# Kernel optimization log

Measured on AMD Instinct MI355X. Metric: run time of the kernel, lower is better.

## Reference

```python
import jax, jax.numpy as jnp
import numpy as np

D = 1024
H = 8          # MHA fallback num_heads
DH = D // H
DFF = 4096     # mlp_ratio * hidden_size
EPS = 1e-6


def _ln(x, g, b):
    mu = jnp.mean(x, axis=-1, keepdims=True)
    var = jnp.mean((x - mu) ** 2, axis=-1, keepdims=True)
    return (x - mu) * jax.lax.rsqrt(var + EPS) * g + b


def setup_inputs() -> dict:
    key = jax.random.key(0)
    ks = jax.random.split(key, 16)
    s = 0.02
    return {
        "x": jax.random.normal(ks[0], (8, 1024, D), jnp.float32),
        "c": jax.random.normal(ks[1], (8, D), jnp.float32),
        # Mamba-block (attention fallback) params
        "m_ada_w": jax.random.normal(ks[2], (D, 3 * D), jnp.float32) * s,
        "m_ada_b": jnp.zeros((3 * D,), jnp.float32),
        "m_norm_g": jnp.ones((D,), jnp.float32),
        "m_norm_b": jnp.zeros((D,), jnp.float32),
        "in_proj_w": jax.random.normal(ks[3], (3 * D, D), jnp.float32) * s,
        "in_proj_b": jnp.zeros((3 * D,), jnp.float32),
        "out_proj_w": jax.random.normal(ks[4], (D, D), jnp.float32) * s,
        "out_proj_b": jnp.zeros((D,), jnp.float32),
        # FeedForward-block params
        "f_ada_w": jax.random.normal(ks[5], (D, 3 * D), jnp.float32) * s,
        "f_ada_b": jnp.zeros((3 * D,), jnp.float32),
        "f_norm_g": jnp.ones((D,), jnp.float32),
        "f_norm_b": jnp.zeros((D,), jnp.float32),
        "w1": jax.random.normal(ks[6], (D, DFF), jnp.float32) * s,
        "b1": jnp.zeros((DFF,), jnp.float32),
        "w2": jax.random.normal(ks[7], (DFF, D), jnp.float32) * s,
        "b2": jnp.zeros((D,), jnp.float32),
    }


def reference(x, c, m_ada_w, m_ada_b, m_norm_g, m_norm_b, in_proj_w, in_proj_b,
              out_proj_w, out_proj_b, f_ada_w, f_ada_b, f_norm_g, f_norm_b,
              w1, b1, w2, b2):
    B, N, _ = x.shape
    # ---- MambaBlock (MHA fallback), dropout = identity (eval) ----
    mod = jax.nn.silu(c) @ m_ada_w + m_ada_b              # (B, 3D)
    shift, scale, gate = jnp.split(mod, 3, axis=-1)
    h = _ln(x, m_norm_g, m_norm_b)
    h = h * (1.0 + scale[:, None, :]) + shift[:, None, :]
    qkv = h @ in_proj_w.T + in_proj_b                      # (B, N, 3D)
    q, k, v = jnp.split(qkv, 3, axis=-1)
    q = q.reshape(B, N, H, DH)
    k = k.reshape(B, N, H, DH)
    v = v.reshape(B, N, H, DH)
    scores = jnp.einsum("bqhd,bkhd->bhqk", q, k) / np.sqrt(DH).astype(np.float32)
    attn = jax.nn.softmax(scores, axis=-1)
    o = jnp.einsum("bhqk,bkhd->bqhd", attn, v).reshape(B, N, D)
    o = o @ out_proj_w.T + out_proj_b
    x = x + gate[:, None, :] * o
    # ---- FeedForward block ----
    mod2 = jax.nn.silu(c) @ f_ada_w + f_ada_b
    shift2, scale2, gate2 = jnp.split(mod2, 3, axis=-1)
    h = _ln(x, f_norm_g, f_norm_b)
    h = h * (1.0 + scale2[:, None, :]) + shift2[:, None, :]
    h = jax.nn.gelu(h @ w1 + b1, approximate=False) @ w2 + b2
    return x + gate2[:, None, :] * h
```

## Files before the change

### kernel.cpp

```cpp
#include <hip/hip_runtime.h>

typedef __bf16 bf16x8 __attribute__((ext_vector_type(8)));
typedef float f32x4 __attribute__((ext_vector_type(4)));

__device__ __forceinline__ unsigned short f2bf(float f) {
    unsigned int u = __float_as_uint(f);
    unsigned int r = (u + 0x7FFFu + ((u >> 16) & 1u)) >> 16;
    return (unsigned short)r;
}

__device__ __forceinline__ void gload16(const void* g, void* l) {
    __builtin_amdgcn_global_load_lds(
        (const __attribute__((address_space(1))) unsigned int*)g,
        (__attribute__((address_space(3))) unsigned int*)l, 16, 0, 0);
}

__device__ __forceinline__ void barrier_raw() {
    asm volatile("" ::: "memory");
    __builtin_amdgcn_s_barrier();
    asm volatile("" ::: "memory");
}

__device__ __forceinline__ void vmwait0() {
    asm volatile("s_waitcnt vmcnt(0)" ::: "memory");
}

__device__ __forceinline__ float gelu_fast(float u) {
    float z = 1.595769122f * u + 0.071354816f * u * u * u;
    return u / (1.f + __expf(-z));
}

__global__ __launch_bounds__(256) void f2b4(const float* __restrict__ in,
                                            unsigned short* __restrict__ out) {
    size_t i = ((size_t)blockIdx.x * 256 + threadIdx.x) * 4;
    float4 v = *(const float4*)(in + i);
    ushort4 o;
    o.x = f2bf(v.x); o.y = f2bf(v.y); o.z = f2bf(v.z); o.w = f2bf(v.w);
    *(ushort4*)(out + i) = o;
}

__global__ __launch_bounds__(256) void transpose_f2b(const float* __restrict__ in,
                                                     unsigned short* __restrict__ out,
                                                     int R, int C) {
    __shared__ float tile[32][33];
    int r0 = blockIdx.y * 32, c0 = blockIdx.x * 32;
    int tx = threadIdx.x & 31, ty = threadIdx.x >> 5;
#pragma unroll
    for (int i = 0; i < 4; i++) {
        int r = ty + i * 8;
        tile[r][tx] = in[(size_t)(r0 + r) * C + c0 + tx];
    }
    __syncthreads();
#pragma unroll
    for (int i = 0; i < 4; i++) {
        int r = ty + i * 8;
        out[(size_t)(c0 + r) * R + r0 + tx] = f2bf(tile[tx][r]);
    }
}

__global__ __launch_bounds__(256) void ada_mod_part(const float* __restrict__ c,
                                                    const float* __restrict__ W,
                                                    float* __restrict__ partial) {
    __shared__ float sc[8 * 64];
    int kc = blockIdx.y * 64;
    for (int i = threadIdx.x; i < 512; i += 256) {
        int b = i >> 6, k = i & 63;
        float cv = c[b * 1024 + kc + k];
        sc[i] = cv / (1.f + __expf(-cv));
    }
    __syncthreads();
    int j = blockIdx.x * 256 + threadIdx.x;
    float acc[8] = {0, 0, 0, 0, 0, 0, 0, 0};
    for (int k = 0; k < 64; k++) {
        float w = W[(size_t)(kc + k) * 3072 + j];
#pragma unroll
        for (int b = 0; b < 8; b++) acc[b] += sc[b * 64 + k] * w;
    }
#pragma unroll
    for (int b = 0; b < 8; b++) partial[((size_t)blockIdx.y * 8 + b) * 3072 + j] = acc[b];
}

__global__ __launch_bounds__(256) void ada_reduce(const float* __restrict__ partial,
                                                  const float* __restrict__ bias,
                                                  float* __restrict__ out) {
    int idx = blockIdx.x * 256 + threadIdx.x;
    int b = idx / 3072;
    int jj = idx - b * 3072;
    float s = bias[jj];
#pragma unroll
    for (int ch = 0; ch < 16; ch++) s += partial[((size_t)ch * 8 + b) * 3072 + jj];
    out[idx] = s;
}

__global__ __launch_bounds__(256) void ln_mod_kernel(const float* __restrict__ x,
                                                     const float* __restrict__ gamma,
                                                     const float* __restrict__ beta,
                                                     const float* __restrict__ mods,
                                                     unsigned short* __restrict__ out) {
    int row = blockIdx.x;
    int b = row >> 10;
    float4 v = ((const float4*)(x + (size_t)row * 1024))[threadIdx.x];
    float s = v.x + v.y + v.z + v.w;
    float s2 = v.x * v.x + v.y * v.y + v.z * v.z + v.w * v.w;
#pragma unroll
    for (int d = 1; d < 64; d <<= 1) { s += __shfl_xor(s, d); s2 += __shfl_xor(s2, d); }
    __shared__ float red[8];
    int lane = threadIdx.x & 63, wid = threadIdx.x >> 6;
    if (lane == 0) { red[wid] = s; red[4 + wid] = s2; }
    __syncthreads();
    float S = red[0] + red[1] + red[2] + red[3];
    float S2 = red[4] + red[5] + red[6] + red[7];
    float mu = S * (1.f / 1024.f);
    float var = S2 * (1.f / 1024.f) - mu * mu;
    float rs = rsqrtf(var + 1e-6f);
    const float* mrow = mods + b * 3072;
    int j0 = threadIdx.x * 4;
    float hv[4] = {v.x, v.y, v.z, v.w};
    ushort4 o;
    unsigned short* op = (unsigned short*)&o;
#pragma unroll
    for (int i = 0; i < 4; i++) {
        int j = j0 + i;
        float hh = (hv[i] - mu) * rs * gamma[j] + beta[j];
        hh = hh * (1.f + mrow[1024 + j]) + mrow[j];
        op[i] = f2bf(hh);
    }
    *(ushort4*)(out + (size_t)row * 1024 + j0) = o;
}

template <int EP>
__global__ __launch_bounds__(256, 2) void gemmw(const unsigned short* __restrict__ A,
                                                const unsigned short* __restrict__ Bt,
                                                int N, int K, int nx,
                                                const float* __restrict__ bias,
                                                unsigned short* __restrict__ outb,
                                                unsigned short* __restrict__ vt) {
    constexpr int AE = 128 * 32;
    constexpr int BE = 256 * 32;
    extern __shared__ __align__(16) char smem[];
    __bf16* As = (__bf16*)smem;
    __bf16* Bs = As + 3 * AE;

    int tid = threadIdx.x, lane = tid & 63, wid = tid >> 6;
    int t = lane & 15, g = lane >> 4;
    int xk2 = ((t >> 1) & 3) * 8;

    int nwg = gridDim.x, chunk = nwg >> 3;
    int swz = (blockIdx.x & 7) * chunk + (blockIdx.x >> 3);
    int bx = swz % nx, by = swz / nx;
    int rowA0 = by * 128, colB0 = bx * 256;

    int rin = tid >> 2, cblk = tid & 3;
    int scol = (cblk ^ ((rin >> 1) & 3)) * 8;

    auto stage = [&](int nb, int kt) {
        int k0 = kt << 5;
        gload16(A + (size_t)(rowA0 + rin) * K + k0 + scol, As + nb * AE + tid * 8);
        gload16(A + (size_t)(rowA0 + 64 + rin) * K + k0 + scol,
                As + nb * AE + 2048 + tid * 8);
#pragma unroll
        for (int sl = 0; sl < 4; sl++)
            gload16(Bt + (size_t)(colB0 + sl * 64 + rin) * K + k0 + scol,
                    Bs + nb * BE + sl * 2048 + tid * 8);
    };

    f32x4 acc[8][4];
#pragma unroll
    for (int m = 0; m < 8; m++)
#pragma unroll
        for (int n = 0; n < 4; n++) acc[m][n] = (f32x4){0.f, 0.f, 0.f, 0.f};

    int NT = K >> 5;
    stage(0, 0);
    if (NT > 1) {
        stage(1, 1);
        asm volatile("s_waitcnt vmcnt(6)" ::: "memory");
    } else {
        vmwait0();
    }
    barrier_raw();

    int cur = 0, tgt = 2;
#pragma unroll 1
    for (int kt = 0; kt < NT; ++kt) {
        bool deep = (kt + 2) < NT;
        bool more = (kt + 1) < NT;
        if (deep) stage(tgt, kt + 2);
        const __bf16* Ac = As + cur * AE;
        const __bf16* Bc = Bs + cur * BE;

        bf16x8 b[4];
#pragma unroll
        for (int n = 0; n < 4; n++)
            b[n] = *(const bf16x8*)&Bc[(wid * 64 + n * 16 + t) * 32 + ((g * 8) ^ xk2)];

        __builtin_amdgcn_s_setprio(1);
#pragma unroll
        for (int mh = 0; mh < 2; mh++) {
            bf16x8 a[4];
#pragma unroll
            for (int m4 = 0; m4 < 4; m4++)
                a[m4] = *(const bf16x8*)&Ac[(mh * 64 + m4 * 16 + t) * 32 + ((g * 8) ^ xk2)];
#pragma unroll
            for (int m4 = 0; m4 < 4; m4++)
#pragma unroll
                for (int n = 0; n < 4; n++)
                    acc[mh * 4 + m4][n] =
                        __builtin_amdgcn_mfma_f32_16x16x32_bf16(a[m4], b[n], acc[mh * 4 + m4][n], 0, 0, 0);
        }
        __builtin_amdgcn_s_setprio(0);

        if (more) {
            if (deep) {
                asm volatile("s_waitcnt vmcnt(6)" ::: "memory");
            } else {
                vmwait0();
            }
            barrier_raw();
        }
        cur = (cur == 2) ? 0 : cur + 1;
        tgt = (tgt == 2) ? 0 : tgt + 1;
    }

    int col0 = colB0 + wid * 64;
    bool vpart = (EP == 0) && (colB0 >= 2048);
#pragma unroll
    for (int m = 0; m < 8; m++)
#pragma unroll
        for (int n = 0; n < 4; n++) {
            int col = col0 + n * 16 + t;
            if (EP == 0 && vpart) {
                int hcol = col - 2048;
                int hh = hcol >> 7, d = hcol & 127;
                int bb = rowA0 >> 10;
                int ntok = (rowA0 + m * 16 + g * 4) & 1023;
                float bs = bias[col];
                ushort4 vv;
                vv.x = f2bf(acc[m][n][0] + bs);
                vv.y = f2bf(acc[m][n][1] + bs);
                vv.z = f2bf(acc[m][n][2] + bs);
                vv.w = f2bf(acc[m][n][3] + bs);
                *(ushort4*)(vt + (((size_t)(bb * 8 + hh) * 128 + d) * 1024 + ntok)) = vv;
            } else {
#pragma unroll
                for (int r = 0; r < 4; r++) {
                    int row = rowA0 + m * 16 + g * 4 + r;
                    float v = acc[m][n][r];
                    if (EP == 0) {
                        outb[(size_t)row * N + col] = f2bf(v + bias[col]);
                    } else {
                        outb[(size_t)row * N + col] = f2bf(gelu_fast(v + bias[col]));
                    }
                }
            }
        }
}

template <int EP>
__global__ __launch_bounds__(256, 4) void gemmo(const unsigned short* __restrict__ A,
                                                const unsigned short* __restrict__ Bt,
                                                int N, int K, int nx,
                                                const float* __restrict__ bias,
                                                const float* __restrict__ xres,
                                                const float* __restrict__ mods,
                                                float* __restrict__ outf) {
    constexpr int AE = 128 * 32;
    constexpr int BE = 128 * 32;
    extern __shared__ __align__(16) char smem[];
    __bf16* As = (__bf16*)smem;
    __bf16* Bs = As + 3 * AE;

    int tid = threadIdx.x, lane = tid & 63, wid = tid >> 6;
    int wr = wid >> 1, wc = wid & 1;
    int t = lane & 15, g = lane >> 4;
    int xk2 = ((t >> 1) & 3) * 8;

    int nwg = gridDim.x, chunk = nwg >> 3;
    int swz = (blockIdx.x & 7) * chunk + (blockIdx.x >> 3);
    int bx = swz % nx, by = swz / nx;
    int rowA0 = by * 128, colB0 = bx * 128;

    int rin = tid >> 2, cblk = tid & 3;
    int scol = (cblk ^ ((rin >> 1) & 3)) * 8;

    auto stage = [&](int nb, int kt) {
        int k0 = kt << 5;
        gload16(A + (size_t)(rowA0 + rin) * K + k0 + scol, As + nb * AE + tid * 8);
        gload16(A + (size_t)(rowA0 + 64 + rin) * K + k0 + scol,
                As + nb * AE + 2048 + tid * 8);
        gload16(Bt + (size_t)(colB0 + rin) * K + k0 + scol, Bs + nb * BE + tid * 8);
        gload16(Bt + (size_t)(colB0 + 64 + rin) * K + k0 + scol,
                Bs + nb * BE + 2048 + tid * 8);
    };

    f32x4 acc[4][4];
#pragma unroll
    for (int m = 0; m < 4; m++)
#pragma unroll
        for (int n = 0; n < 4; n++) acc[m][n] = (f32x4){0.f, 0.f, 0.f, 0.f};

    int NT = K >> 5;
    stage(0, 0);
    if (NT > 1) {
        stage(1, 1);
        asm volatile("s_waitcnt vmcnt(4)" ::: "memory");
    } else {
        vmwait0();
    }
    barrier_raw();

    int cur = 0, tgt = 2;
#pragma unroll 1
    for (int kt = 0; kt < NT; ++kt) {
        bool deep = (kt + 2) < NT;
        bool more = (kt + 1) < NT;
        if (deep) stage(tgt, kt + 2);
        const __bf16* Ac = As + cur * AE;
        const __bf16* Bc = Bs + cur * BE;

        bf16x8 a[4], b[4];
#pragma unroll
        for (int m = 0; m < 4; m++)
            a[m] = *(const bf16x8*)&Ac[(wr * 64 + m * 16 + t) * 32 + ((g * 8) ^ xk2)];
#pragma unroll
        for (int n = 0; n < 4; n++)
            b[n] = *(const bf16x8*)&Bc[(wc * 64 + n * 16 + t) * 32 + ((g * 8) ^ xk2)];

        __builtin_amdgcn_s_setprio(1);
#pragma unroll
        for (int m = 0; m < 4; m++)
#pragma unroll
            for (int n = 0; n < 4; n++)
                acc[m][n] = __builtin_amdgcn_mfma_f32_16x16x32_bf16(a[m], b[n], acc[m][n], 0, 0, 0);
        __builtin_amdgcn_s_setprio(0);

        if (more) {
            if (deep) {
                asm volatile("s_waitcnt vmcnt(4)" ::: "memory");
            } else {
                vmwait0();
            }
            barrier_raw();
        }
        cur = (cur == 2) ? 0 : cur + 1;
        tgt = (tgt == 2) ? 0 : tgt + 1;
    }

    int row0 = rowA0 + wr * 64, col0 = colB0 + wc * 64;
#pragma unroll
    for (int m = 0; m < 4; m++)
#pragma unroll
        for (int n = 0; n < 4; n++) {
            int col = col0 + n * 16 + t;
#pragma unroll
            for (int r = 0; r < 4; r++) {
                int row = row0 + m * 16 + g * 4 + r;
                float v = acc[m][n][r];
                int bb = row >> 10;
                float gt = mods[bb * 3072 + 2048 + col];
                if (EP == 1) {
                    outf[(size_t)row * 1024 + col] =
                        xres[(size_t)row * 1024 + col] + gt * (v + bias[col]);
                } else {
                    outf[(size_t)row * 1024 + col] += gt * (v + bias[col]);
                }
            }
        }
}

__global__ __launch_bounds__(512, 4) void attn_kernel(const unsigned short* __restrict__ qkv,
                                                      const unsigned short* __restrict__ vt,
                                                      unsigned short* __restrict__ o) {
    extern __shared__ __align__(16) char asmem[];
    __bf16* Ks = (__bf16*)asmem;
    __bf16* Vts = Ks + 2 * 64 * 128;

    int bid = blockIdx.x;
    int logical = (bid & 7) * 64 + (bid >> 3);
    int q0 = (logical & 7) * 128;
    int bh = logical >> 3;
    int b = bh >> 3, h = bh & 7;
    int tid = threadIdx.x, lane = tid & 63, w = tid >> 6;
    int t = lane & 15, g = lane >> 4;
    int swzt = (t & 7) << 4;

    const unsigned short* qbase = qkv + (size_t)(b * 1024) * 3072 + h * 128;
    int qrow = q0 + w * 16 + t;
    bf16x8 qf[4];
#pragma unroll
    for (int ks = 0; ks < 4; ks++)
        qf[ks] = *(const bf16x8*)(qbase + (size_t)qrow * 3072 + ks * 32 + g * 8);

    f32x4 Oa[8];
#pragma unroll
    for (int n = 0; n < 8; n++) Oa[n] = (f32x4){0.f, 0.f, 0.f, 0.f};
    float m_r = -1e30f, l_r = 0.f;
    const float scale = 0.08838834764831845f;

    int krow = tid >> 4;
    int ksrc = (((tid & 15) * 16) ^ ((krow & 7) << 4)) >> 1;
    int vrow = tid >> 3;
    int vsrc = (((tid & 7) * 16) ^ ((vrow & 7) << 4)) >> 1;
    const unsigned short* vtg = vt + (size_t)bh * 128 * 1024;

    auto stage = [&](int buf, int kv0) {
        const unsigned short* kb = qkv + (size_t)(b * 1024 + kv0) * 3072 + 1024 + h * 128;
#pragma unroll
        for (int cc = 0; cc < 2; cc++) {
            gload16(kb + (size_t)(cc * 32 + krow) * 3072 + ksrc,
                    (void*)(Ks + buf * 8192 + cc * 4096 + tid * 8));
            gload16(vtg + (size_t)(cc * 64 + vrow) * 1024 + kv0 + vsrc,
                    (void*)(Vts + buf * 8192 + cc * 4096 + tid * 8));
        }
    };

    stage(0, 0);
    vmwait0();
    barrier_raw();

#pragma unroll 1
    for (int tile = 0; tile < 16; ++tile) {
        int cur = tile & 1;
        bool more = tile < 15;
        if (more) stage(cur ^ 1, (tile + 1) * 64);
        const __bf16* Kc = Ks + cur * 8192;
        const __bf16* Vc = Vts + cur * 8192;

        f32x4 St[4];
#pragma unroll
        for (int n = 0; n < 4; n++) St[n] = (f32x4){0.f, 0.f, 0.f, 0.f};
        __builtin_amdgcn_s_setprio(1);
#pragma unroll
        for (int ks = 0; ks < 4; ks++) {
#pragma unroll
            for (int n = 0; n < 4; n++) {
                bf16x8 kf = *(const bf16x8*)&Kc[(n * 16 + t) * 128 + (((ks * 64 + g * 16) ^ swzt) >> 1)];
                St[n] = __builtin_amdgcn_mfma_f32_16x16x32_bf16(kf, qf[ks], St[n], 0, 0, 0);
            }
        }
        __builtin_amdgcn_s_setprio(0);

        float mx = -1e30f;
#pragma unroll
        for (int n = 0; n < 4; n++)
#pragma unroll
            for (int r = 0; r < 4; r++) mx = fmaxf(mx, St[n][r]);
        mx *= scale;
        mx = fmaxf(mx, __shfl_xor(mx, 16));
        mx = fmaxf(mx, __shfl_xor(mx, 32));
        float mn = fmaxf(m_r, mx);
        float alpha = __expf(m_r - mn);
        m_r = mn;
        float p[4][4];
        float rs = 0.f;
#pragma unroll
        for (int n = 0; n < 4; n++)
#pragma unroll
            for (int r = 0; r < 4; r++) {
                float pv = __expf(St[n][r] * scale - mn);
                p[n][r] = pv;
                rs += pv;
            }
        rs += __shfl_xor(rs, 16);
        rs += __shfl_xor(rs, 32);
        l_r = l_r * alpha + rs;

        unsigned P01[4], P23[4];
#pragma unroll
        for (int n = 0; n < 4; n++) {
            P01[n] = (unsigned)f2bf(p[n][0]) | ((unsigned)f2bf(p[n][1]) << 16);
            P23[n] = (unsigned)f2bf(p[n][2]) | ((unsigned)f2bf(p[n][3]) << 16);
        }

#pragma unroll
        for (int r = 0; r < 4; r++) {
            float ar = __shfl(alpha, (lane & 48) + g * 4 + r);
#pragma unroll
            for (int n2 = 0; n2 < 8; n2++) Oa[n2][r] *= ar;
        }

#pragma unroll
        for (int ks2 = 0; ks2 < 2; ks2++) {
            int e = ks2 * 2, od = ks2 * 2 + 1;
            unsigned s16a = (g < 2) ? P01[e] : P01[od];
            unsigned s16b = (g < 2) ? P23[e] : P23[od];
            unsigned s32a = (g & 1) ? P01[e] : P01[od];
            unsigned s32b = (g & 1) ? P23[e] : P23[od];
            unsigned s48a = (g >= 2) ? P01[e] : P01[od];
            unsigned s48b = (g >= 2) ? P23[e] : P23[od];
            unsigned r16a = __shfl_xor(s16a, 16), r16b = __shfl_xor(s16b, 16);
            unsigned r32a = __shfl_xor(s32a, 32), r32b = __shfl_xor(s32b, 32);
            unsigned r48a = __shfl_xor(s48a, 48), r48b = __shfl_xor(s48b, 48);
            union { unsigned u[4]; bf16x8 v; } pa;
            pa.u[0] = (g == 0) ? P01[e] : (g == 1) ? r48a : (g == 2) ? r32a : r16a;
            pa.u[1] = (g == 0) ? P23[e] : (g == 1) ? r48b : (g == 2) ? r32b : r16b;
            pa.u[2] = (g == 0) ? r16a : (g == 1) ? r32a : (g == 2) ? r48a : P01[od];
            pa.u[3] = (g == 0) ? r16b : (g == 1) ? r32b : (g == 2) ? r48b : P23[od];
            __builtin_amdgcn_s_setprio(1);
#pragma unroll
            for (int n2 = 0; n2 < 8; n2++) {
                bf16x8 vf = *(const bf16x8*)&Vc[(n2 * 16 + t) * 64 + (((ks2 * 64 + g * 16) ^ swzt) >> 1)];
                Oa[n2] = __builtin_amdgcn_mfma_f32_16x16x32_bf16(pa.v, vf, Oa[n2], 0, 0, 0);
            }
            __builtin_amdgcn_s_setprio(0);
        }

        if (more) {
            vmwait0();
            barrier_raw();
        }
    }

#pragma unroll
    for (int r = 0; r < 4; r++) {
        float lq = __shfl(l_r, (lane & 48) + g * 4 + r);
        float inv = 1.f / lq;
        int orow = q0 + w * 16 + g * 4 + r;
#pragma unroll
        for (int n2 = 0; n2 < 8; n2++)
            o[(size_t)(b * 1024 + orow) * 1024 + h * 128 + n2 * 16 + t] = f2bf(Oa[n2][r] * inv);
    }
}

extern "C" void kernel_launch(void* const* d_in, const int* in_sizes, int n_in,
                              void* d_out, int out_size, void* d_ws, size_t ws_size,
                              hipStream_t stream) {
    const float* x          = (const float*)d_in[0];
    const float* c          = (const float*)d_in[1];
    const float* m_ada_w    = (const float*)d_in[2];
    const float* m_ada_b    = (const float*)d_in[3];
    const float* m_norm_g   = (const float*)d_in[4];
    const float* m_norm_b   = (const float*)d_in[5];
    const float* in_proj_w  = (const float*)d_in[6];
    const float* in_proj_b  = (const float*)d_in[7];
    const float* out_proj_w = (const float*)d_in[8];
    const float* out_proj_b = (const float*)d_in[9];
    const float* f_ada_w    = (const float*)d_in[10];
    const float* f_ada_b    = (const float*)d_in[11];
    const float* f_norm_g   = (const float*)d_in[12];
    const float* f_norm_b   = (const float*)d_in[13];
    const float* w1         = (const float*)d_in[14];
    const float* b1         = (const float*)d_in[15];
    const float* w2         = (const float*)d_in[16];
    const float* b2         = (const float*)d_in[17];
    float* out = (float*)d_out;
    char* ws = (char*)d_ws;

    unsigned short* Wq   = (unsigned short*)(ws + 0);
    unsigned short* Wo   = (unsigned short*)(ws + 6291456);
    unsigned short* vt   = (unsigned short*)(ws + 8388608);
    unsigned short* W1t  = (unsigned short*)(ws + 8388608);
    unsigned short* W2t  = (unsigned short*)(ws + 16777216);
    float*          modm = (float*)(ws + 25165824);
    float*          modf = (float*)(ws + 25264128);
    unsigned short* hbuf = (unsigned short*)(ws + 25362432);
    float*          part = (float*)(ws + 25362432);
    float*          part2= (float*)(ws + 25362432 + 2097152);
    unsigned short* qkv  = (unsigned short*)(ws + 42139648);
    unsigned short* obuf = (unsigned short*)(ws + 92471296);
    unsigned short* h2   = (unsigned short*)(ws + 42139648);

    hipFuncSetAttribute((const void*)&gemmw<0>, hipFuncAttributeMaxDynamicSharedMemorySize, 73728);
    hipFuncSetAttribute((const void*)&gemmw<2>, hipFuncAttributeMaxDynamicSharedMemorySize, 73728);
    hipFuncSetAttribute((const void*)&gemmo<1>, hipFuncAttributeMaxDynamicSharedMemorySize, 49152);
    hipFuncSetAttribute((const void*)&gemmo<3>, hipFuncAttributeMaxDynamicSharedMemorySize, 49152);
    hipFuncSetAttribute((const void*)&attn_kernel, hipFuncAttributeMaxDynamicSharedMemorySize, 65536);

    hipLaunchKernelGGL(ada_mod_part, dim3(12, 16), dim3(256), 0, stream, c, m_ada_w, part);
    hipLaunchKernelGGL(ada_mod_part, dim3(12, 16), dim3(256), 0, stream, c, f_ada_w, part2);
    hipLaunchKernelGGL(ada_reduce, dim3(96), dim3(256), 0, stream, part, m_ada_b, modm);
    hipLaunchKernelGGL(ada_reduce, dim3(96), dim3(256), 0, stream, part2, f_ada_b, modf);

    hipLaunchKernelGGL(f2b4, dim3(3072), dim3(256), 0, stream, in_proj_w, Wq);
    hipLaunchKernelGGL(f2b4, dim3(1024), dim3(256), 0, stream, out_proj_w, Wo);

    hipLaunchKernelGGL(ln_mod_kernel, dim3(8192), dim3(256), 0, stream, x, m_norm_g, m_norm_b, modm, hbuf);
    hipLaunchKernelGGL(HIP_KERNEL_NAME(gemmw<0>), dim3(768), dim3(256), 73728, stream,
                       hbuf, Wq, 3072, 1024, 12, in_proj_b, qkv, vt);
    hipLaunchKernelGGL(attn_kernel, dim3(512), dim3(512), 65536, stream, qkv, vt, obuf);
    hipLaunchKernelGGL(HIP_KERNEL_NAME(gemmo<1>), dim3(512), dim3(256), 49152, stream,
                       obuf, Wo, 1024, 1024, 8, out_proj_b, x, modm, out);

    hipLaunchKernelGGL(transpose_f2b, dim3(128, 32), dim3(256), 0, stream, w1, W1t, 1024, 4096);
    hipLaunchKernelGGL(transpose_f2b, dim3(32, 128), dim3(256), 0, stream, w2, W2t, 4096, 1024);

    hipLaunchKernelGGL(ln_mod_kernel, dim3(8192), dim3(256), 0, stream, out, f_norm_g, f_norm_b, modf, hbuf);
    hipLaunchKernelGGL(HIP_KERNEL_NAME(gemmw<2>), dim3(1024), dim3(256), 73728, stream,
                       hbuf, W1t, 4096, 1024, 16, b1, h2, (unsigned short*)nullptr);
    hipLaunchKernelGGL(HIP_KERNEL_NAME(gemmo<3>), dim3(512), dim3(256), 49152, stream,
                       h2, W2t, 1024, 4096, 8, b2, (const float*)nullptr, modf, out);
}
```

Measured before the change: 386.6 us.

## Replace wide GEMM with 8-wave 256x256 tile, ping-pong staged schedule

Replaces the 256-thread 128x256 GEMM used for the QKV and W1 projections with a 512-thread kernel that computes 256x256 output tiles with BK=64 and double-buffered LDS (128 KB). Each k-step is split into four quarter-MFMA phases whose fragment loads and next-tile global loads are interleaved between barriers, with priority bumps, to overlap memory traffic with matrix math. The larger tile doubles data reuse per LDS byte, but it uses the full LDS budget, which limits occupancy to one block per CU. It also adds many barriers per k-step, and the grid shrinks to 384/512 blocks, which can hurt load balance.

```diff
diff --git a/kernel.cpp b/kernel.cpp
--- a/kernel.cpp
+++ b/kernel.cpp
@@ -23,6 +23,11 @@
 
 __device__ __forceinline__ void vmwait0() {
     asm volatile("s_waitcnt vmcnt(0)" ::: "memory");
+}
+
+__device__ __forceinline__ void lgkm0_fence() {
+    asm volatile("s_waitcnt lgkmcnt(0)" ::: "memory");
+    __builtin_amdgcn_sched_barrier(0);
 }
 
 __device__ __forceinline__ float gelu_fast(float u) {
@@ -129,40 +134,44 @@
 }
 
 template <int EP>
-__global__ __launch_bounds__(256, 2) void gemmw(const unsigned short* __restrict__ A,
+__global__ __launch_bounds__(512, 2) void gemm8(const unsigned short* __restrict__ A,
                                                 const unsigned short* __restrict__ Bt,
                                                 int N, int K, int nx,
                                                 const float* __restrict__ bias,
                                                 unsigned short* __restrict__ outb,
                                                 unsigned short* __restrict__ vt) {
-    constexpr int AE = 128 * 32;
-    constexpr int BE = 256 * 32;
+    constexpr int TE = 256 * 64;
     extern __shared__ __align__(16) char smem[];
     __bf16* As = (__bf16*)smem;
-    __bf16* Bs = As + 3 * AE;
+    __bf16* Bs = As + 2 * TE;
 
     int tid = threadIdx.x, lane = tid & 63, wid = tid >> 6;
+    int wr = wid >> 2, wc = wid & 3;
     int t = lane & 15, g = lane >> 4;
-    int xk2 = ((t >> 1) & 3) * 8;
+    int xk = (t & 7) * 8;
 
     int nwg = gridDim.x, chunk = nwg >> 3;
     int swz = (blockIdx.x & 7) * chunk + (blockIdx.x >> 3);
     int bx = swz % nx, by = swz / nx;
-    int rowA0 = by * 128, colB0 = bx * 256;
-
-    int rin = tid >> 2, cblk = tid & 3;
-    int scol = (cblk ^ ((rin >> 1) & 3)) * 8;
-
-    auto stage = [&](int nb, int kt) {
-        int k0 = kt << 5;
-        gload16(A + (size_t)(rowA0 + rin) * K + k0 + scol, As + nb * AE + tid * 8);
-        gload16(A + (size_t)(rowA0 + 64 + rin) * K + k0 + scol,
-                As + nb * AE + 2048 + tid * 8);
-#pragma unroll
-        for (int sl = 0; sl < 4; sl++)
-            gload16(Bt + (size_t)(colB0 + sl * 64 + rin) * K + k0 + scol,
-                    Bs + nb * BE + sl * 2048 + tid * 8);
+    int rowA0 = by * 256, colB0 = bx * 256;
+
+    int rin = tid >> 3, cblk = tid & 7;
+    int scol = (cblk ^ (rin & 7)) * 8;
+
+    auto stageA = [&](int d, int h, int kt) {
+        int k0 = kt << 6;
+        const unsigned short* src = A + (size_t)(rowA0 + h * 128 + rin) * K + k0 + scol;
+        __bf16* dst = As + d * TE + (h * 128 + rin) * 64 + cblk * 8;
+        gload16(src, dst);
+        gload16(src + (size_t)64 * K, dst + 4096);
     };
+    auto stageB = [&](int d, int h, int kt) {
+        int k0 = kt << 6;
+        const unsigned short* src = Bt + (size_t)(colB0 + h * 128 + rin) * K + k0 + scol;
+        __bf16* dst = Bs + d * TE + (h * 128 + rin) * 64 + cblk * 8;
+        gload16(src, dst);
+        gload16(src + (size_t)64 * K, dst + 4096);
+    };
 
     f32x4 acc[8][4];
 #pragma unroll
@@ -170,59 +179,104 @@
 #pragma unroll
         for (int n = 0; n < 4; n++) acc[m][n] = (f32x4){0.f, 0.f, 0.f, 0.f};
 
-    int NT = K >> 5;
-    stage(0, 0);
+    int NT = K >> 6;
+    stageA(0, 0, 0); stageA(0, 1, 0); stageB(0, 0, 0); stageB(0, 1, 0);
     if (NT > 1) {
-        stage(1, 1);
+        stageA(1, 0, 1); stageA(1, 1, 1); stageB(1, 0, 1);
         asm volatile("s_waitcnt vmcnt(6)" ::: "memory");
     } else {
         vmwait0();
     }
     barrier_raw();
 
-    int cur = 0, tgt = 2;
 #pragma unroll 1
     for (int kt = 0; kt < NT; ++kt) {
-        bool deep = (kt + 2) < NT;
-        bool more = (kt + 1) < NT;
-        if (deep) stage(tgt, kt + 2);
-        const __bf16* Ac = As + cur * AE;
-        const __bf16* Bc = Bs + cur * BE;
-
-        bf16x8 b[4];
-#pragma unroll
-        for (int n = 0; n < 4; n++)
-            b[n] = *(const bf16x8*)&Bc[(wid * 64 + n * 16 + t) * 32 + ((g * 8) ^ xk2)];
-
+        int d = kt & 1, dn = d ^ 1;
+        const __bf16* Ab = As + d * TE;
+        const __bf16* Bb = Bs + d * TE;
+        bool s1 = kt + 1 < NT, s2 = kt + 2 < NT;
+
+        auto LDA = [&](int mh, int m4, int ks) -> bf16x8 {
+            int R = wr * 128 + mh * 64 + m4 * 16 + t;
+            return *(const bf16x8*)&Ab[R * 64 + ((ks * 32 + g * 8) ^ xk)];
+        };
+        auto LDB = [&](int nh, int n2, int ks) -> bf16x8 {
+            int R = wc * 64 + nh * 32 + n2 * 16 + t;
+            return *(const bf16x8*)&Bb[R * 64 + ((ks * 32 + g * 8) ^ xk)];
+        };
+
+        bf16x8 a0[4][2], a1[4][2], b0[2][2], b1[2][2];
+
+#pragma unroll
+        for (int m4 = 0; m4 < 4; m4++) { a0[m4][0] = LDA(0, m4, 0); a0[m4][1] = LDA(0, m4, 1); }
+#pragma unroll
+        for (int n2 = 0; n2 < 2; n2++) { b0[n2][0] = LDB(0, n2, 0); b0[n2][1] = LDB(0, n2, 1); }
+        if (s1) stageB(dn, 1, kt + 1);
+        barrier_raw();
+        lgkm0_fence();
         __builtin_amdgcn_s_setprio(1);
 #pragma unroll
-        for (int mh = 0; mh < 2; mh++) {
-            bf16x8 a[4];
-#pragma unroll
-            for (int m4 = 0; m4 < 4; m4++)
-                a[m4] = *(const bf16x8*)&Ac[(mh * 64 + m4 * 16 + t) * 32 + ((g * 8) ^ xk2)];
-#pragma unroll
-            for (int m4 = 0; m4 < 4; m4++)
-#pragma unroll
-                for (int n = 0; n < 4; n++)
-                    acc[mh * 4 + m4][n] =
-                        __builtin_amdgcn_mfma_f32_16x16x32_bf16(a[m4], b[n], acc[mh * 4 + m4][n], 0, 0, 0);
-        }
+        for (int m4 = 0; m4 < 4; m4++)
+#pragma unroll
+            for (int n2 = 0; n2 < 2; n2++)
+#pragma unroll
+                for (int ks = 0; ks < 2; ks++)
+                    acc[m4][n2] = __builtin_amdgcn_mfma_f32_16x16x32_bf16(a0[m4][ks], b0[n2][ks], acc[m4][n2], 0, 0, 0);
         __builtin_amdgcn_s_setprio(0);
-
-        if (more) {
-            if (deep) {
+        barrier_raw();
+
+#pragma unroll
+        for (int m4 = 0; m4 < 4; m4++) { a1[m4][0] = LDA(1, m4, 0); a1[m4][1] = LDA(1, m4, 1); }
+        barrier_raw();
+        lgkm0_fence();
+        __builtin_amdgcn_s_setprio(1);
+#pragma unroll
+        for (int m4 = 0; m4 < 4; m4++)
+#pragma unroll
+            for (int n2 = 0; n2 < 2; n2++)
+#pragma unroll
+                for (int ks = 0; ks < 2; ks++)
+                    acc[4 + m4][n2] = __builtin_amdgcn_mfma_f32_16x16x32_bf16(a1[m4][ks], b0[n2][ks], acc[4 + m4][n2], 0, 0, 0);
+        __builtin_amdgcn_s_setprio(0);
+        barrier_raw();
+
+#pragma unroll
+        for (int n2 = 0; n2 < 2; n2++) { b1[n2][0] = LDB(1, n2, 0); b1[n2][1] = LDB(1, n2, 1); }
+        if (s2) stageA(d, 0, kt + 2);
+        barrier_raw();
+        lgkm0_fence();
+        __builtin_amdgcn_s_setprio(1);
+#pragma unroll
+        for (int m4 = 0; m4 < 4; m4++)
+#pragma unroll
+            for (int n2 = 0; n2 < 2; n2++)
+#pragma unroll
+                for (int ks = 0; ks < 2; ks++)
+                    acc[4 + m4][2 + n2] = __builtin_amdgcn_mfma_f32_16x16x32_bf16(a1[m4][ks], b1[n2][ks], acc[4 + m4][2 + n2], 0, 0, 0);
+        __builtin_amdgcn_s_setprio(0);
+        barrier_raw();
+
+        if (s2) { stageA(d, 1, kt + 2); stageB(d, 0, kt + 2); }
+        __builtin_amdgcn_s_setprio(1);
+#pragma unroll
+        for (int m4 = 0; m4 < 4; m4++)
+#pragma unroll
+            for (int n2 = 0; n2 < 2; n2++)
+#pragma unroll
+                for (int ks = 0; ks < 2; ks++)
+                    acc[m4][2 + n2] = __builtin_amdgcn_mfma_f32_16x16x32_bf16(a0[m4][ks], b1[n2][ks], acc[m4][2 + n2], 0, 0, 0);
+        __builtin_amdgcn_s_setprio(0);
+        if (s1) {
+            if (s2) {
                 asm volatile("s_waitcnt vmcnt(6)" ::: "memory");
             } else {
-                vmwait0();
+                asm volatile("s_waitcnt vmcnt(0)" ::: "memory");
             }
             barrier_raw();
         }
-        cur = (cur == 2) ? 0 : cur + 1;
-        tgt = (tgt == 2) ? 0 : tgt + 1;
-    }
-
-    int col0 = colB0 + wid * 64;
+    }
+
+    int col0 = colB0 + wc * 64;
     bool vpart = (EP == 0) && (colB0 >= 2048);
 #pragma unroll
     for (int m = 0; m < 8; m++)
@@ -231,20 +285,21 @@
             int col = col0 + n * 16 + t;
             if (EP == 0 && vpart) {
                 int hcol = col - 2048;
-                int hh = hcol >> 7, d = hcol & 127;
-                int bb = rowA0 >> 10;
-                int ntok = (rowA0 + m * 16 + g * 4) & 1023;
+                int hh = hcol >> 7, dd = hcol & 127;
+                int row0 = rowA0 + wr * 128 + m * 16 + g * 4;
+                int bb = row0 >> 10;
+                int ntok = row0 & 1023;
                 float bs = bias[col];
                 ushort4 vv;
                 vv.x = f2bf(acc[m][n][0] + bs);
                 vv.y = f2bf(acc[m][n][1] + bs);
                 vv.z = f2bf(acc[m][n][2] + bs);
                 vv.w = f2bf(acc[m][n][3] + bs);
-                *(ushort4*)(vt + (((size_t)(bb * 8 + hh) * 128 + d) * 1024 + ntok)) = vv;
+                *(ushort4*)(vt + (((size_t)(bb * 8 + hh) * 128 + dd) * 1024 + ntok)) = vv;
             } else {
 #pragma unroll
                 for (int r = 0; r < 4; r++) {
-                    int row = rowA0 + m * 16 + g * 4 + r;
+                    int row = rowA0 + wr * 128 + m * 16 + g * 4 + r;
                     float v = acc[m][n][r];
                     if (EP == 0) {
                         outb[(size_t)row * N + col] = f2bf(v + bias[col]);
@@ -560,8 +615,8 @@
     unsigned short* obuf = (unsigned short*)(ws + 92471296);
     unsigned short* h2   = (unsigned short*)(ws + 42139648);
 
-    hipFuncSetAttribute((const void*)&gemmw<0>, hipFuncAttributeMaxDynamicSharedMemorySize, 73728);
-    hipFuncSetAttribute((const void*)&gemmw<2>, hipFuncAttributeMaxDynamicSharedMemorySize, 73728);
+    hipFuncSetAttribute((const void*)&gemm8<0>, hipFuncAttributeMaxDynamicSharedMemorySize, 131072);
+    hipFuncSetAttribute((const void*)&gemm8<2>, hipFuncAttributeMaxDynamicSharedMemorySize, 131072);
     hipFuncSetAttribute((const void*)&gemmo<1>, hipFuncAttributeMaxDynamicSharedMemorySize, 49152);
     hipFuncSetAttribute((const void*)&gemmo<3>, hipFuncAttributeMaxDynamicSharedMemorySize, 49152);
     hipFuncSetAttribute((const void*)&attn_kernel, hipFuncAttributeMaxDynamicSharedMemorySize, 65536);
@@ -575,7 +630,7 @@
     hipLaunchKernelGGL(f2b4, dim3(1024), dim3(256), 0, stream, out_proj_w, Wo);
 
     hipLaunchKernelGGL(ln_mod_kernel, dim3(8192), dim3(256), 0, stream, x, m_norm_g, m_norm_b, modm, hbuf);
-    hipLaunchKernelGGL(HIP_KERNEL_NAME(gemmw<0>), dim3(768), dim3(256), 73728, stream,
+    hipLaunchKernelGGL(HIP_KERNEL_NAME(gemm8<0>), dim3(384), dim3(512), 131072, stream,
                        hbuf, Wq, 3072, 1024, 12, in_proj_b, qkv, vt);
     hipLaunchKernelGGL(attn_kernel, dim3(512), dim3(512), 65536, stream, qkv, vt, obuf);
     hipLaunchKernelGGL(HIP_KERNEL_NAME(gemmo<1>), dim3(512), dim3(256), 49152, stream,
@@ -585,7 +640,7 @@
     hipLaunchKernelGGL(transpose_f2b, dim3(32, 128), dim3(256), 0, stream, w2, W2t, 4096, 1024);
 
     hipLaunchKernelGGL(ln_mod_kernel, dim3(8192), dim3(256), 0, stream, out, f_norm_g, f_norm_b, modf, hbuf);
-    hipLaunchKernelGGL(HIP_KERNEL_NAME(gemmw<2>), dim3(1024), dim3(256), 73728, stream,
+    hipLaunchKernelGGL(HIP_KERNEL_NAME(gemm8<2>), dim3(512), dim3(512), 131072, stream,
                        hbuf, W1t, 4096, 1024, 16, b1, h2, (unsigned short*)nullptr);
     hipLaunchKernelGGL(HIP_KERNEL_NAME(gemmo<3>), dim3(512), dim3(256), 49152, stream,
                        h2, W2t, 1024, 4096, 8, b2, (const float*)nullptr, modf, out);
```

Result: no change. 382.3 us (-1.1%).
